# Kernel tuning notes

Hardware: AMD Instinct MI355X
Metric: run time of the kernel (lower is better)

Reference implementation:

```python
import jax, jax.numpy as jnp
import numpy as np

B, N = 8192, 512
WEIGHT_THRESHOLD = 0.0
EPS = 1e-5


def setup_inputs() -> dict:
    key = jax.random.key(0)
    k1, k2, k3 = jax.random.split(key, 3)
    src_points = jax.random.normal(k1, (B, N, 3), dtype=jnp.float32)
    tgt_points = jax.random.normal(k2, (B, N, 3), dtype=jnp.float32)
    weights = jax.random.uniform(k3, (B, N), dtype=jnp.float32)
    return {"src_points": src_points, "tgt_points": tgt_points, "weights": weights}


def _weighted_procrustes(src, tgt, w):
    # threshold + normalize weights  (B, N)
    w = jnp.where(w < WEIGHT_THRESHOLD, jnp.zeros_like(w), w)
    w = w / (jnp.sum(w, axis=1, keepdims=True) + EPS)
    w3 = w[..., None]                                   # (B, N, 1)
    # weighted centroids (B, 1, 3)
    src_c = jnp.sum(w3 * src, axis=1, keepdims=True)
    tgt_c = jnp.sum(w3 * tgt, axis=1, keepdims=True)
    src0 = src - src_c
    tgt0 = tgt - tgt_c
    # weighted covariance H = src0^T (w * tgt0)  -> (B, 3, 3)
    H = jnp.einsum("bni,bnj->bij", src0, w3 * tgt0)
    U, S, Vh = jnp.linalg.svd(H)
    V = jnp.swapaxes(Vh, -1, -2)
    Ut = jnp.swapaxes(U, -1, -2)
    # reflection correction: diag(1, 1, sign(det(V U^T)))
    det = jnp.linalg.det(jnp.matmul(V, Ut))             # (B,)
    ones = jnp.ones((src.shape[0], 2), dtype=src.dtype)
    d = jnp.concatenate([ones, jnp.sign(det)[:, None]], axis=1)  # (B, 3)
    R = jnp.einsum("bij,bj,bjk->bik", V, d, Ut)         # (B, 3, 3)
    t = tgt_c[:, 0, :] - jnp.einsum("bij,bj->bi", R, src_c[:, 0, :])  # (B, 3)
    return R, t


def reference(src_points, tgt_points, weights):
    return _weighted_procrustes(src_points, tgt_points, weights)
```

## Files before the change

### kernel.cpp

```cpp
#include <hip/hip_runtime.h>

#define NPTS 512
#define BLOCK 256
#define XPS 68

__global__ __launch_bounds__(BLOCK) void wproc_moments(
    const float* __restrict__ src,
    const float* __restrict__ tgt,
    const float* __restrict__ wts,
    float* __restrict__ ws)
{
    const int wave = threadIdx.x >> 6;
    const int lane = threadIdx.x & 63;
    const int b = blockIdx.x * 4 + wave;

    const float* sb = src + (size_t)b * (NPTS * 3);
    const float* tb = tgt + (size_t)b * (NPTS * 3);
    const float* wb = wts + (size_t)b * NPTS;

    float acc[16];
    #pragma unroll
    for (int i = 0; i < 16; ++i) acc[i] = 0.f;

    #pragma unroll
    for (int k = 0; k < 8; ++k) {
        const int p = lane + 64 * k;
        float w = wb[p];
        w = (w < 0.f) ? 0.f : w;
        const float sx = sb[3 * p + 0], sy = sb[3 * p + 1], sz = sb[3 * p + 2];
        const float tx = tb[3 * p + 0], ty = tb[3 * p + 1], tz = tb[3 * p + 2];
        acc[0] += w;
        acc[1] += w * sx; acc[2] += w * sy; acc[3] += w * sz;
        acc[4] += w * tx; acc[5] += w * ty; acc[6] += w * tz;
        const float wsx = w * sx, wsy = w * sy, wsz = w * sz;
        acc[7]  += wsx * tx; acc[8]  += wsx * ty; acc[9]  += wsx * tz;
        acc[10] += wsy * tx; acc[11] += wsy * ty; acc[12] += wsy * tz;
        acc[13] += wsz * tx; acc[14] += wsz * ty; acc[15] += wsz * tz;
    }

    __shared__ float xp[4][16][XPS];
    #pragma unroll
    for (int m = 0; m < 16; ++m) xp[wave][m][lane] = acc[m];

    {
        const int m = lane & 15, q = lane >> 4;
        const float4* row = (const float4*)&xp[wave][m][0] + 4 * q;
        float4 a0 = row[0], a1 = row[1], a2 = row[2], a3 = row[3];
        a0.x += a1.x; a0.y += a1.y; a0.z += a1.z; a0.w += a1.w;
        a2.x += a3.x; a2.y += a3.y; a2.z += a3.z; a2.w += a3.w;
        a0.x += a2.x; a0.y += a2.y; a0.z += a2.z; a0.w += a2.w;
        float v = (a0.x + a0.y) + (a0.z + a0.w);
        v += __shfl_xor(v, 16, 64);
        v += __shfl_xor(v, 32, 64);
        if (q == 0) ws[(size_t)b * 16 + m] = v;
    }
}

__global__ __launch_bounds__(BLOCK) void wproc_solve(
    const float* __restrict__ ws,
    float* __restrict__ out,
    int B)
{
    const int b = blockIdx.x * BLOCK + threadIdx.x;
    if (b >= B) return;

    double m[16];
    #pragma unroll
    for (int i = 0; i < 16; ++i) m[i] = (double)ws[(size_t)b * 16 + i];

    const double T = m[0] + 1e-5;
    const double f = 2.0 - m[0] / T;
    const double cs[3] = { m[1] / T, m[2] / T, m[3] / T };
    const double ct[3] = { m[4] / T, m[5] / T, m[6] / T };
    double H[3][3];
    for (int i = 0; i < 3; ++i)
        for (int j = 0; j < 3; ++j)
            H[i][j] = m[7 + i * 3 + j] / T - f * cs[i] * ct[j];

    double A[3][3];
    for (int i = 0; i < 3; ++i)
        for (int j = 0; j < 3; ++j)
            A[i][j] = H[0][i] * H[0][j] + H[1][i] * H[1][j] + H[2][i] * H[2][j];

    double V[3][3] = { {1, 0, 0}, {0, 1, 0}, {0, 0, 1} };
    for (int sweep = 0; sweep < 5; ++sweep) {
        for (int pair = 0; pair < 3; ++pair) {
            const int p = (pair == 2) ? 1 : 0;
            const int q = (pair == 0) ? 1 : 2;
            const double apq = A[p][q];
            if (apq == 0.0) continue;
            const double theta = (A[q][q] - A[p][p]) / (2.0 * apq);
            const double tt = ((theta >= 0.0) ? 1.0 : -1.0)
                            / (fabs(theta) + sqrt(theta * theta + 1.0));
            const double c = 1.0 / sqrt(tt * tt + 1.0);
            const double sn = tt * c;
            for (int k = 0; k < 3; ++k) {
                const double akp = A[k][p], akq = A[k][q];
                A[k][p] = c * akp - sn * akq;
                A[k][q] = sn * akp + c * akq;
            }
            for (int k = 0; k < 3; ++k) {
                const double apk = A[p][k], aqk = A[q][k];
                A[p][k] = c * apk - sn * aqk;
                A[q][k] = sn * apk + c * aqk;
            }
            for (int k = 0; k < 3; ++k) {
                const double vkp = V[k][p], vkq = V[k][q];
                V[k][p] = c * vkp - sn * vkq;
                V[k][q] = sn * vkp + c * vkq;
            }
        }
    }

    const double lam[3] = { A[0][0], A[1][1], A[2][2] };
    int i0 = 0, i1 = 1, i2 = 2;
    if (lam[i0] < lam[i1]) { int tmp = i0; i0 = i1; i1 = tmp; }
    if (lam[i0] < lam[i2]) { int tmp = i0; i0 = i2; i2 = tmp; }
    if (lam[i1] < lam[i2]) { int tmp = i1; i1 = i2; i2 = tmp; }

    const double v1[3] = { V[0][i0], V[1][i0], V[2][i0] };
    const double v2[3] = { V[0][i1], V[1][i1], V[2][i1] };
    const double v3[3] = { v1[1] * v2[2] - v1[2] * v2[1],
                           v1[2] * v2[0] - v1[0] * v2[2],
                           v1[0] * v2[1] - v1[1] * v2[0] };

    double u1[3], u2[3], u3[3];
    for (int i = 0; i < 3; ++i)
        u1[i] = H[i][0] * v1[0] + H[i][1] * v1[1] + H[i][2] * v1[2];
    double n1 = sqrt(u1[0] * u1[0] + u1[1] * u1[1] + u1[2] * u1[2]);
    n1 = (n1 > 1e-30) ? n1 : 1e-30;
    for (int i = 0; i < 3; ++i) u1[i] /= n1;

    for (int i = 0; i < 3; ++i)
        u2[i] = H[i][0] * v2[0] + H[i][1] * v2[1] + H[i][2] * v2[2];
    const double d12 = u1[0] * u2[0] + u1[1] * u2[1] + u1[2] * u2[2];
    for (int i = 0; i < 3; ++i) u2[i] -= d12 * u1[i];
    double n2 = sqrt(u2[0] * u2[0] + u2[1] * u2[1] + u2[2] * u2[2]);
    n2 = (n2 > 1e-30) ? n2 : 1e-30;
    for (int i = 0; i < 3; ++i) u2[i] /= n2;

    u3[0] = u1[1] * u2[2] - u1[2] * u2[1];
    u3[1] = u1[2] * u2[0] - u1[0] * u2[2];
    u3[2] = u1[0] * u2[1] - u1[1] * u2[0];

    double R[3][3];
    for (int i = 0; i < 3; ++i)
        for (int j = 0; j < 3; ++j)
            R[i][j] = v1[i] * u1[j] + v2[i] * u2[j] + v3[i] * u3[j];

    double tv[3];
    for (int i = 0; i < 3; ++i)
        tv[i] = ct[i] - (R[i][0] * cs[0] + R[i][1] * cs[1] + R[i][2] * cs[2]);

    float* outR = out + (size_t)b * 9;
    for (int i = 0; i < 3; ++i)
        for (int j = 0; j < 3; ++j)
            outR[i * 3 + j] = (float)R[i][j];
    float* outT = out + (size_t)B * 9 + (size_t)b * 3;
    for (int i = 0; i < 3; ++i) outT[i] = (float)tv[i];
}

extern "C" void kernel_launch(void* const* d_in, const int* in_sizes, int n_in,
                              void* d_out, int out_size, void* d_ws, size_t ws_size,
                              hipStream_t stream) {
    const float* src = (const float*)d_in[0];
    const float* tgt = (const float*)d_in[1];
    const float* wts = (const float*)d_in[2];
    float* out = (float*)d_out;
    float* ws = (float*)d_ws;
    const int B = out_size / 12;

    wproc_moments<<<B / 4, BLOCK, 0, stream>>>(src, tgt, wts, ws);
    wproc_solve<<<(B + BLOCK - 1) / BLOCK, BLOCK, 0, stream>>>(ws, out, B);
}
```

Before: 148.1 us.

## Fuse moments and SVD solve into one kernel with float4 vectorized loads

Merges the moment-reduction kernel and the per-batch 3x3 SVD solve into a single kernel. Each wave reduces into shared memory and lane 0 then runs the double-precision Jacobi solve and writes R and t directly, removing the second launch and the workspace round trip. Input loads change from scalar strided reads to float4 reads of 4 points per lane, and launch bounds now request 4 blocks per CU. The risk is that the serial fp64 solve on one lane per wave now stalls the block and adds register pressure in the streaming kernel.

```diff
diff --git a/kernel.cpp b/kernel.cpp
--- a/kernel.cpp
+++ b/kernel.cpp
@@ -4,41 +4,56 @@
 #define BLOCK 256
 #define XPS 68
 
-__global__ __launch_bounds__(BLOCK) void wproc_moments(
+__global__ __launch_bounds__(BLOCK, 4) void wproc_fused(
     const float* __restrict__ src,
     const float* __restrict__ tgt,
     const float* __restrict__ wts,
-    float* __restrict__ ws)
+    float* __restrict__ out,
+    int B)
 {
     const int wave = threadIdx.x >> 6;
     const int lane = threadIdx.x & 63;
     const int b = blockIdx.x * 4 + wave;
 
-    const float* sb = src + (size_t)b * (NPTS * 3);
-    const float* tb = tgt + (size_t)b * (NPTS * 3);
-    const float* wb = wts + (size_t)b * NPTS;
+    const float4* sb4 = (const float4*)(src + (size_t)b * (NPTS * 3));
+    const float4* tb4 = (const float4*)(tgt + (size_t)b * (NPTS * 3));
+    const float4* wb4 = (const float4*)(wts + (size_t)b * NPTS);
 
     float acc[16];
     #pragma unroll
     for (int i = 0; i < 16; ++i) acc[i] = 0.f;
 
     #pragma unroll
-    for (int k = 0; k < 8; ++k) {
-        const int p = lane + 64 * k;
-        float w = wb[p];
-        w = (w < 0.f) ? 0.f : w;
-        const float sx = sb[3 * p + 0], sy = sb[3 * p + 1], sz = sb[3 * p + 2];
-        const float tx = tb[3 * p + 0], ty = tb[3 * p + 1], tz = tb[3 * p + 2];
-        acc[0] += w;
-        acc[1] += w * sx; acc[2] += w * sy; acc[3] += w * sz;
-        acc[4] += w * tx; acc[5] += w * ty; acc[6] += w * tz;
-        const float wsx = w * sx, wsy = w * sy, wsz = w * sz;
-        acc[7]  += wsx * tx; acc[8]  += wsx * ty; acc[9]  += wsx * tz;
-        acc[10] += wsy * tx; acc[11] += wsy * ty; acc[12] += wsy * tz;
-        acc[13] += wsz * tx; acc[14] += wsz * ty; acc[15] += wsz * tz;
+    for (int k = 0; k < 2; ++k) {
+        const int c3 = 3 * lane + 192 * k;
+        float4 sv0 = sb4[c3 + 0], sv1 = sb4[c3 + 1], sv2 = sb4[c3 + 2];
+        float4 tv0 = tb4[c3 + 0], tv1 = tb4[c3 + 1], tv2 = tb4[c3 + 2];
+        float4 wv  = wb4[lane + 64 * k];
+
+        const float sf[12] = { sv0.x, sv0.y, sv0.z, sv0.w, sv1.x, sv1.y,
+                               sv1.z, sv1.w, sv2.x, sv2.y, sv2.z, sv2.w };
+        const float tf[12] = { tv0.x, tv0.y, tv0.z, tv0.w, tv1.x, tv1.y,
+                               tv1.z, tv1.w, tv2.x, tv2.y, tv2.z, tv2.w };
+        const float wf[4] = { wv.x, wv.y, wv.z, wv.w };
+
+        #pragma unroll
+        for (int j = 0; j < 4; ++j) {
+            float w = wf[j];
+            w = (w < 0.f) ? 0.f : w;
+            const float sx = sf[3 * j + 0], sy = sf[3 * j + 1], sz = sf[3 * j + 2];
+            const float tx = tf[3 * j + 0], ty = tf[3 * j + 1], tz = tf[3 * j + 2];
+            acc[0] += w;
+            acc[1] += w * sx; acc[2] += w * sy; acc[3] += w * sz;
+            acc[4] += w * tx; acc[5] += w * ty; acc[6] += w * tz;
+            const float wsx = w * sx, wsy = w * sy, wsz = w * sz;
+            acc[7]  += wsx * tx; acc[8]  += wsx * ty; acc[9]  += wsx * tz;
+            acc[10] += wsy * tx; acc[11] += wsy * ty; acc[12] += wsy * tz;
+            acc[13] += wsz * tx; acc[14] += wsz * ty; acc[15] += wsz * tz;
+        }
     }
 
     __shared__ float xp[4][16][XPS];
+    __shared__ float red[4][16];
     #pragma unroll
     for (int m = 0; m < 16; ++m) xp[wave][m][lane] = acc[m];
 
@@ -52,112 +67,105 @@
         float v = (a0.x + a0.y) + (a0.z + a0.w);
         v += __shfl_xor(v, 16, 64);
         v += __shfl_xor(v, 32, 64);
-        if (q == 0) ws[(size_t)b * 16 + m] = v;
+        if (q == 0) red[wave][m] = v;
     }
-}
 
-__global__ __launch_bounds__(BLOCK) void wproc_solve(
-    const float* __restrict__ ws,
-    float* __restrict__ out,
-    int B)
-{
-    const int b = blockIdx.x * BLOCK + threadIdx.x;
-    if (b >= B) return;
+    if (lane == 0) {
+        double m[16];
+        #pragma unroll
+        for (int i = 0; i < 16; ++i) m[i] = (double)red[wave][i];
 
-    double m[16];
-    #pragma unroll
-    for (int i = 0; i < 16; ++i) m[i] = (double)ws[(size_t)b * 16 + i];
+        const double T = m[0] + 1e-5;
+        const double f = 2.0 - m[0] / T;
+        const double cs[3] = { m[1] / T, m[2] / T, m[3] / T };
+        const double ct[3] = { m[4] / T, m[5] / T, m[6] / T };
+        double H[3][3];
+        for (int i = 0; i < 3; ++i)
+            for (int j = 0; j < 3; ++j)
+                H[i][j] = m[7 + i * 3 + j] / T - f * cs[i] * ct[j];
 
-    const double T = m[0] + 1e-5;
-    const double f = 2.0 - m[0] / T;
-    const double cs[3] = { m[1] / T, m[2] / T, m[3] / T };
-    const double ct[3] = { m[4] / T, m[5] / T, m[6] / T };
-    double H[3][3];
-    for (int i = 0; i < 3; ++i)
-        for (int j = 0; j < 3; ++j)
-            H[i][j] = m[7 + i * 3 + j] / T - f * cs[i] * ct[j];
+        double A[3][3];
+        for (int i = 0; i < 3; ++i)
+            for (int j = 0; j < 3; ++j)
+                A[i][j] = H[0][i] * H[0][j] + H[1][i] * H[1][j] + H[2][i] * H[2][j];
 
-    double A[3][3];
-    for (int i = 0; i < 3; ++i)
-        for (int j = 0; j < 3; ++j)
-            A[i][j] = H[0][i] * H[0][j] + H[1][i] * H[1][j] + H[2][i] * H[2][j];
-
-    double V[3][3] = { {1, 0, 0}, {0, 1, 0}, {0, 0, 1} };
-    for (int sweep = 0; sweep < 5; ++sweep) {
-        for (int pair = 0; pair < 3; ++pair) {
-            const int p = (pair == 2) ? 1 : 0;
-            const int q = (pair == 0) ? 1 : 2;
-            const double apq = A[p][q];
-            if (apq == 0.0) continue;
-            const double theta = (A[q][q] - A[p][p]) / (2.0 * apq);
-            const double tt = ((theta >= 0.0) ? 1.0 : -1.0)
-                            / (fabs(theta) + sqrt(theta * theta + 1.0));
-            const double c = 1.0 / sqrt(tt * tt + 1.0);
-            const double sn = tt * c;
-            for (int k = 0; k < 3; ++k) {
-                const double akp = A[k][p], akq = A[k][q];
-                A[k][p] = c * akp - sn * akq;
-                A[k][q] = sn * akp + c * akq;
-            }
-            for (int k = 0; k < 3; ++k) {
-                const double apk = A[p][k], aqk = A[q][k];
-                A[p][k] = c * apk - sn * aqk;
-                A[q][k] = sn * apk + c * aqk;
-            }
-            for (int k = 0; k < 3; ++k) {
-                const double vkp = V[k][p], vkq = V[k][q];
-                V[k][p] = c * vkp - sn * vkq;
-                V[k][q] = sn * vkp + c * vkq;
+        double V[3][3] = { {1, 0, 0}, {0, 1, 0}, {0, 0, 1} };
+        for (int sweep = 0; sweep < 5; ++sweep) {
+            for (int pair = 0; pair < 3; ++pair) {
+                const int p = (pair == 2) ? 1 : 0;
+                const int q = (pair == 0) ? 1 : 2;
+                const double apq = A[p][q];
+                if (apq == 0.0) continue;
+                const double theta = (A[q][q] - A[p][p]) / (2.0 * apq);
+                const double tt = ((theta >= 0.0) ? 1.0 : -1.0)
+                                / (fabs(theta) + sqrt(theta * theta + 1.0));
+                const double c = 1.0 / sqrt(tt * tt + 1.0);
+                const double sn = tt * c;
+                for (int k = 0; k < 3; ++k) {
+                    const double akp = A[k][p], akq = A[k][q];
+                    A[k][p] = c * akp - sn * akq;
+                    A[k][q] = sn * akp + c * akq;
+                }
+                for (int k = 0; k < 3; ++k) {
+                    const double apk = A[p][k], aqk = A[q][k];
+                    A[p][k] = c * apk - sn * aqk;
+                    A[q][k] = sn * apk + c * aqk;
+                }
+                for (int k = 0; k < 3; ++k) {
+                    const double vkp = V[k][p], vkq = V[k][q];
+                    V[k][p] = c * vkp - sn * vkq;
+                    V[k][q] = sn * vkp + c * vkq;
+                }
             }
         }
+
+        const double lam[3] = { A[0][0], A[1][1], A[2][2] };
+        int i0 = 0, i1 = 1, i2 = 2;
+        if (lam[i0] < lam[i1]) { int tmp = i0; i0 = i1; i1 = tmp; }
+        if (lam[i0] < lam[i2]) { int tmp = i0; i0 = i2; i2 = tmp; }
+        if (lam[i1] < lam[i2]) { int tmp = i1; i1 = i2; i2 = tmp; }
+
+        const double v1[3] = { V[0][i0], V[1][i0], V[2][i0] };
+        const double v2[3] = { V[0][i1], V[1][i1], V[2][i1] };
+        const double v3[3] = { v1[1] * v2[2] - v1[2] * v2[1],
+                               v1[2] * v2[0] - v1[0] * v2[2],
+                               v1[0] * v2[1] - v1[1] * v2[0] };
+
+        double u1[3], u2[3], u3[3];
+        for (int i = 0; i < 3; ++i)
+            u1[i] = H[i][0] * v1[0] + H[i][1] * v1[1] + H[i][2] * v1[2];
+        double n1 = sqrt(u1[0] * u1[0] + u1[1] * u1[1] + u1[2] * u1[2]);
+        n1 = (n1 > 1e-30) ? n1 : 1e-30;
+        for (int i = 0; i < 3; ++i) u1[i] /= n1;
+
+        for (int i = 0; i < 3; ++i)
+            u2[i] = H[i][0] * v2[0] + H[i][1] * v2[1] + H[i][2] * v2[2];
+        const double d12 = u1[0] * u2[0] + u1[1] * u2[1] + u1[2] * u2[2];
+        for (int i = 0; i < 3; ++i) u2[i] -= d12 * u1[i];
+        double n2 = sqrt(u2[0] * u2[0] + u2[1] * u2[1] + u2[2] * u2[2]);
+        n2 = (n2 > 1e-30) ? n2 : 1e-30;
+        for (int i = 0; i < 3; ++i) u2[i] /= n2;
+
+        u3[0] = u1[1] * u2[2] - u1[2] * u2[1];
+        u3[1] = u1[2] * u2[0] - u1[0] * u2[2];
+        u3[2] = u1[0] * u2[1] - u1[1] * u2[0];
+
+        double R[3][3];
+        for (int i = 0; i < 3; ++i)
+            for (int j = 0; j < 3; ++j)
+                R[i][j] = v1[i] * u1[j] + v2[i] * u2[j] + v3[i] * u3[j];
+
+        double tv[3];
+        for (int i = 0; i < 3; ++i)
+            tv[i] = ct[i] - (R[i][0] * cs[0] + R[i][1] * cs[1] + R[i][2] * cs[2]);
+
+        float* outR = out + (size_t)b * 9;
+        for (int i = 0; i < 3; ++i)
+            for (int j = 0; j < 3; ++j)
+                outR[i * 3 + j] = (float)R[i][j];
+        float* outT = out + (size_t)B * 9 + (size_t)b * 3;
+        for (int i = 0; i < 3; ++i) outT[i] = (float)tv[i];
     }
-
-    const double lam[3] = { A[0][0], A[1][1], A[2][2] };
-    int i0 = 0, i1 = 1, i2 = 2;
-    if (lam[i0] < lam[i1]) { int tmp = i0; i0 = i1; i1 = tmp; }
-    if (lam[i0] < lam[i2]) { int tmp = i0; i0 = i2; i2 = tmp; }
-    if (lam[i1] < lam[i2]) { int tmp = i1; i1 = i2; i2 = tmp; }
-
-    const double v1[3] = { V[0][i0], V[1][i0], V[2][i0] };
-    const double v2[3] = { V[0][i1], V[1][i1], V[2][i1] };
-    const double v3[3] = { v1[1] * v2[2] - v1[2] * v2[1],
-                           v1[2] * v2[0] - v1[0] * v2[2],
-                           v1[0] * v2[1] - v1[1] * v2[0] };
-
-    double u1[3], u2[3], u3[3];
-    for (int i = 0; i < 3; ++i)
-        u1[i] = H[i][0] * v1[0] + H[i][1] * v1[1] + H[i][2] * v1[2];
-    double n1 = sqrt(u1[0] * u1[0] + u1[1] * u1[1] + u1[2] * u1[2]);
-    n1 = (n1 > 1e-30) ? n1 : 1e-30;
-    for (int i = 0; i < 3; ++i) u1[i] /= n1;
-
-    for (int i = 0; i < 3; ++i)
-        u2[i] = H[i][0] * v2[0] + H[i][1] * v2[1] + H[i][2] * v2[2];
-    const double d12 = u1[0] * u2[0] + u1[1] * u2[1] + u1[2] * u2[2];
-    for (int i = 0; i < 3; ++i) u2[i] -= d12 * u1[i];
-    double n2 = sqrt(u2[0] * u2[0] + u2[1] * u2[1] + u2[2] * u2[2]);
-    n2 = (n2 > 1e-30) ? n2 : 1e-30;
-    for (int i = 0; i < 3; ++i) u2[i] /= n2;
-
-    u3[0] = u1[1] * u2[2] - u1[2] * u2[1];
-    u3[1] = u1[2] * u2[0] - u1[0] * u2[2];
-    u3[2] = u1[0] * u2[1] - u1[1] * u2[0];
-
-    double R[3][3];
-    for (int i = 0; i < 3; ++i)
-        for (int j = 0; j < 3; ++j)
-            R[i][j] = v1[i] * u1[j] + v2[i] * u2[j] + v3[i] * u3[j];
-
-    double tv[3];
-    for (int i = 0; i < 3; ++i)
-        tv[i] = ct[i] - (R[i][0] * cs[0] + R[i][1] * cs[1] + R[i][2] * cs[2]);
-
-    float* outR = out + (size_t)b * 9;
-    for (int i = 0; i < 3; ++i)
-        for (int j = 0; j < 3; ++j)
-            outR[i * 3 + j] = (float)R[i][j];
-    float* outT = out + (size_t)B * 9 + (size_t)b * 3;
-    for (int i = 0; i < 3; ++i) outT[i] = (float)tv[i];
 }
 
 extern "C" void kernel_launch(void* const* d_in, const int* in_sizes, int n_in,
@@ -167,9 +175,7 @@
     const float* tgt = (const float*)d_in[1];
     const float* wts = (const float*)d_in[2];
     float* out = (float*)d_out;
-    float* ws = (float*)d_ws;
     const int B = out_size / 12;
 
-    wproc_moments<<<B / 4, BLOCK, 0, stream>>>(src, tgt, wts, ws);
-    wproc_solve<<<(B + BLOCK - 1) / BLOCK, BLOCK, 0, stream>>>(ws, out, B);
+    wproc_fused<<<B / 4, BLOCK, 0, stream>>>(src, tgt, wts, out, B);
 }
```

Result: slower. 172.5 us (+16.4%).
